# Performance work log

Hardware: AMD Instinct MI355X
Metric: run time of the kernel (lower is better)

Reference implementation:

```python
import jax, jax.numpy as jnp
import numpy as np

B, S, D, H = 8, 1024, 1024, 16
DK = D // H  # 64


def setup_inputs() -> dict:
    key = jax.random.key(0)
    ks = jax.random.split(key, 12)
    def w(k):
        return (jax.random.normal(k, (D, D), dtype=jnp.float32) * 0.02)
    def b(k):
        return (jax.random.normal(k, (D,), dtype=jnp.float32) * 0.02)
    return {
        "q": jax.random.normal(ks[0], (B, S, D), dtype=jnp.float32),
        "k": jax.random.normal(ks[1], (B, S, D), dtype=jnp.float32),
        "v": jax.random.normal(ks[2], (B, S, D), dtype=jnp.float32),
        "mask": jax.random.randint(ks[3], (B, 1, S, S), 0, 2, dtype=jnp.int32),
        "WQ_w": w(ks[4]), "WQ_b": b(ks[5]),
        "WK_w": w(ks[6]), "WK_b": b(ks[7]),
        "WV_w": w(ks[8]), "WV_b": b(ks[9]),
        "WO_w": w(ks[10]), "WO_b": b(ks[11]),
    }


def reference(q, k, v, mask, WQ_w, WQ_b, WK_w, WK_b, WV_w, WV_b, WO_w, WO_b):
    # nn.Linear: y = x @ W.T + b
    Q = (q @ WQ_w.T + WQ_b).reshape(B, S, H, DK)
    K = (k @ WK_w.T + WK_b).reshape(B, S, H, DK)
    V = (v @ WV_w.T + WV_b).reshape(B, S, H, DK)
    # scores: [B, H, Sq, Sk]
    scores = jnp.einsum("bqhd,bkhd->bhqk", Q, K) / jnp.sqrt(jnp.float32(DK))
    scores = jnp.where(mask == 0, jnp.float32(-1e9), scores)
    attn = jax.nn.softmax(scores, axis=-1)
    # dropout p=0.0 -> identity
    out = jnp.einsum("bhqk,bkhd->bqhd", attn, V).reshape(B, S, D)
    return out @ WO_w.T + WO_b
```

## Files before the change

### kernel.cpp

```cpp
#include <hip/hip_runtime.h>
#include <math.h>

typedef __bf16 bf16;
typedef __bf16 bf16x8 __attribute__((ext_vector_type(8)));
typedef __bf16 bf16x4 __attribute__((ext_vector_type(4)));
typedef float f32x2 __attribute__((ext_vector_type(2)));
typedef float f32x4 __attribute__((ext_vector_type(4)));
typedef float f32x8 __attribute__((ext_vector_type(8)));
typedef float f32x16 __attribute__((ext_vector_type(16)));
typedef int i32x2 __attribute__((ext_vector_type(2)));
typedef int i32x4 __attribute__((ext_vector_type(4)));

constexpr int B_ = 8, S_ = 1024, D_ = 1024, H_ = 16, DK_ = 64;
constexpr int M_ = B_ * S_;
constexpr size_t A8 = (size_t)1 << 23;
constexpr size_t W1 = (size_t)1 << 20;
constexpr float QSCALE = 0.18033688011112042f;

#if __has_builtin(__builtin_amdgcn_exp2f)
#define EXP2F(x) __builtin_amdgcn_exp2f(x)
#else
#define EXP2F(x) exp2f(x)
#endif
#if __has_builtin(__builtin_amdgcn_rcpf)
#define RCPF(x) __builtin_amdgcn_rcpf(x)
#else
#define RCPF(x) (1.0f / (x))
#endif

#define GAS(p) ((const __attribute__((address_space(1))) void*)(p))
#define LAS(p) ((__attribute__((address_space(3))) void*)(p))

__device__ __forceinline__ float xor32f(float v, int bpidx) {
    return __builtin_bit_cast(float,
        __builtin_amdgcn_ds_bpermute(bpidx, __builtin_bit_cast(int, v)));
}
__device__ __forceinline__ int xor32i(int v, int bpidx) {
    return __builtin_amdgcn_ds_bpermute(bpidx, v);
}
__device__ __forceinline__ int pack_bf16(bf16 lo, bf16 hi) {
    return (int)(unsigned)__builtin_bit_cast(unsigned short, lo)
         | ((int)(unsigned)__builtin_bit_cast(unsigned short, hi) << 16);
}

struct F4Q { f32x4 a, b, c, d; };

__global__ __launch_bounds__(256) void cvt_all(
    const float* __restrict__ q, const float* __restrict__ k,
    const float* __restrict__ v, const float* __restrict__ w0,
    const float* __restrict__ w1, const float* __restrict__ w2,
    const float* __restrict__ w3, bf16* __restrict__ dst)
{
    size_t e = ((size_t)blockIdx.x * 256 + threadIdx.x) * 8;
    const float* src;
    size_t off;
    if (e < 3 * A8) {
        int t = (int)(e >> 23);
        src = (t == 0) ? q : (t == 1) ? k : v;
        off = e & (A8 - 1);
    } else {
        size_t ew = e - 3 * A8;
        int t = (int)(ew >> 20);
        src = (t == 0) ? w0 : (t == 1) ? w1 : (t == 2) ? w2 : w3;
        off = ew & (W1 - 1);
    }
    float4 a = *(const float4*)(src + off);
    float4 b = *(const float4*)(src + off + 4);
    bf16x8 o = { (bf16)a.x, (bf16)a.y, (bf16)a.z, (bf16)a.w,
                 (bf16)b.x, (bf16)b.y, (bf16)b.z, (bf16)b.w };
    *(bf16x8*)(dst + e) = o;
}

__global__ __launch_bounds__(256) void mask_cvt(
    const int* __restrict__ mask, float* __restrict__ mf)
{
    const int bx = blockIdx.x;
    const int kt = bx & 15, qt = (bx >> 4) & 7, b = bx >> 7;
    const int tid = threadIdx.x;
    const int w = tid >> 6, lane = tid & 63;
    const int hi = lane >> 5, l31 = lane & 31;
    const int q = qt * 128 + w * 32 + l31;

    const int* src = mask + ((size_t)b << 20) + (size_t)q * 1024 + kt * 64 + hi * 4;
    float* dst = mf + (size_t)bx * 8192 + w * 2048 + lane * 4;
#pragma unroll
    for (int blk = 0; blk < 2; ++blk)
#pragma unroll
        for (int rr = 0; rr < 4; ++rr) {
            int4 m = *(const int4*)(src + blk * 32 + rr * 8);
            f32x4 o = { m.x ? 0.f : -1e9f, m.y ? 0.f : -1e9f,
                        m.z ? 0.f : -1e9f, m.w ? 0.f : -1e9f };
            *(f32x4*)(dst + (blk * 4 + rr) * 256) = o;
        }
}

__global__ __launch_bounds__(256) void qkv_gemm(
    const bf16* __restrict__ qb, const bf16* __restrict__ kb,
    const bf16* __restrict__ vb, const bf16* __restrict__ wq,
    const bf16* __restrict__ wk, const bf16* __restrict__ wv,
    const float* __restrict__ bq, const float* __restrict__ bk,
    const float* __restrict__ bv, bf16* __restrict__ Qp,
    bf16* __restrict__ Kp, bf16* __restrict__ Vp, float qscale)
{
    constexpr int K = 1024;
    __shared__ bf16 As[128 * 32];
    __shared__ bf16 Bs[128 * 32];

    const int bid = blockIdx.x;
    const int which = bid >> 9;
    const int gb = bid & 511;
    const bf16* X = which == 0 ? qb : which == 1 ? kb : vb;
    const bf16* W = which == 0 ? wq : which == 1 ? wk : wv;
    const float* bias = which == 0 ? bq : which == 1 ? bk : bv;
    bf16* outp = which == 0 ? Qp : which == 1 ? Kp : Vp;
    const float oscale = which == 0 ? qscale : 1.0f;

    const int tid  = threadIdx.x;
    const int lane = tid & 63;
    const int w    = tid >> 6;
    const int wm   = w & 1, wn = w >> 1;
    const int quad = lane >> 4, l15 = lane & 15;
    const int bm = (gb & 63) * 128, bn = (gb >> 6) * 128;

    f32x4 acc[4][4];
#pragma unroll
    for (int i = 0; i < 4; ++i)
#pragma unroll
        for (int j = 0; j < 4; ++j)
#pragma unroll
            for (int r = 0; r < 4; ++r) acc[i][j][r] = 0.f;

    const int lrow = lane >> 2;
    const int lcol = (lane & 3) * 8;

    for (int k0 = 0; k0 < K; k0 += 32) {
        __syncthreads();
#pragma unroll
        for (int i = 0; i < 2; ++i) {
            const int rbase = w * 16 + i * 64;
            __builtin_amdgcn_global_load_lds(
                GAS(X + (size_t)(bm + rbase + lrow) * K + k0 + lcol),
                LAS(As + rbase * 32), 16, 0, 0);
            __builtin_amdgcn_global_load_lds(
                GAS(W + (size_t)(bn + rbase + lrow) * K + k0 + lcol),
                LAS(Bs + rbase * 32), 16, 0, 0);
        }
        __syncthreads();

        bf16x8 a[4], b[4];
#pragma unroll
        for (int i = 0; i < 4; ++i)
            a[i] = *(const bf16x8*)(As + (wm * 64 + i * 16 + l15) * 32 + quad * 8);
#pragma unroll
        for (int j = 0; j < 4; ++j)
            b[j] = *(const bf16x8*)(Bs + (wn * 64 + j * 16 + l15) * 32 + quad * 8);
#pragma unroll
        for (int i = 0; i < 4; ++i)
#pragma unroll
            for (int j = 0; j < 4; ++j)
                acc[i][j] = __builtin_amdgcn_mfma_f32_16x16x32_bf16(
                    a[i], b[j], acc[i][j], 0, 0, 0);
    }

#pragma unroll
    for (int i = 0; i < 4; ++i) {
#pragma unroll
        for (int j = 0; j < 4; ++j) {
            const int n = bn + wn * 64 + j * 16 + l15;
            const float bs = bias[n];
            if (which == 2) {
                const int m0 = bm + wm * 64 + i * 16 + quad * 4;
                const int bb = m0 >> 10, s0 = m0 & 1023;
                const int h = n >> 6, dk = n & 63;
                bf16x4 o;
#pragma unroll
                for (int r = 0; r < 4; ++r) o[r] = (bf16)(acc[i][j][r] + bs);
                *(bf16x4*)(outp + (((size_t)(bb * 16 + h) * 64 + dk) << 10) + s0) = o;
            } else {
#pragma unroll
                for (int r = 0; r < 4; ++r) {
                    const int m = bm + wm * 64 + i * 16 + quad * 4 + r;
                    const int bb = m >> 10, s = m & 1023;
                    const int h = n >> 6, dk = n & 63;
                    outp[(((size_t)(bb * 16 + h)) * 1024 + s) * 64 + dk] =
                        (bf16)((acc[i][j][r] + bs) * oscale);
                }
            }
        }
    }
}

__global__ __launch_bounds__(256) void gemm_out(
    const bf16* __restrict__ X, const bf16* __restrict__ W,
    const float* __restrict__ bias, float* __restrict__ outv)
{
    constexpr int K = 1024;
    __shared__ bf16 As[128 * 32];
    __shared__ bf16 Bs[128 * 32];

    const int tid  = threadIdx.x;
    const int lane = tid & 63;
    const int w    = tid >> 6;
    const int wm   = w & 1, wn = w >> 1;
    const int quad = lane >> 4, l15 = lane & 15;
    const int bm = blockIdx.x * 128, bn = blockIdx.y * 128;

    f32x4 acc[4][4];
#pragma unroll
    for (int i = 0; i < 4; ++i)
#pragma unroll
        for (int j = 0; j < 4; ++j)
#pragma unroll
            for (int r = 0; r < 4; ++r) acc[i][j][r] = 0.f;

    const int lrow = lane >> 2;
    const int lcol = (lane & 3) * 8;

    for (int k0 = 0; k0 < K; k0 += 32) {
        __syncthreads();
#pragma unroll
        for (int i = 0; i < 2; ++i) {
            const int rbase = w * 16 + i * 64;
            __builtin_amdgcn_global_load_lds(
                GAS(X + (size_t)(bm + rbase + lrow) * K + k0 + lcol),
                LAS(As + rbase * 32), 16, 0, 0);
            __builtin_amdgcn_global_load_lds(
                GAS(W + (size_t)(bn + rbase + lrow) * K + k0 + lcol),
                LAS(Bs + rbase * 32), 16, 0, 0);
        }
        __syncthreads();

        bf16x8 a[4], b[4];
#pragma unroll
        for (int i = 0; i < 4; ++i)
            a[i] = *(const bf16x8*)(As + (wm * 64 + i * 16 + l15) * 32 + quad * 8);
#pragma unroll
        for (int j = 0; j < 4; ++j)
            b[j] = *(const bf16x8*)(Bs + (wn * 64 + j * 16 + l15) * 32 + quad * 8);
#pragma unroll
        for (int i = 0; i < 4; ++i)
#pragma unroll
            for (int j = 0; j < 4; ++j)
                acc[i][j] = __builtin_amdgcn_mfma_f32_16x16x32_bf16(
                    a[i], b[j], acc[i][j], 0, 0, 0);
    }

#pragma unroll
    for (int i = 0; i < 4; ++i)
#pragma unroll
        for (int j = 0; j < 4; ++j) {
            const int n = bn + wn * 64 + j * 16 + l15;
            const float bs = bias[n];
#pragma unroll
            for (int r = 0; r < 4; ++r) {
                const int m = bm + wm * 64 + i * 16 + quad * 4 + r;
                outv[(size_t)m * 1024 + n] = acc[i][j][r] + bs;
            }
        }
}

__global__ __launch_bounds__(256) void attn_mfma(
    const bf16* __restrict__ Q, const bf16* __restrict__ Kt,
    const bf16* __restrict__ Vt, const float* __restrict__ mf,
    bf16* __restrict__ out)
{
    __shared__ bf16 smem[2 * 2 * 4096];

    const int tid  = threadIdx.x;
    const int lane = tid & 63;
    const int w    = tid >> 6;
    const int hi   = lane >> 5, l31 = lane & 31;

    const int wid = (blockIdx.x & 7) * 128 + (blockIdx.x >> 3);
    const int qt = wid & 7;
    const int h  = (wid >> 3) & 15;
    const int b  = wid >> 7;

    const bf16* Qg  = Q + ((size_t)((b * H_ + h) * S_) + qt * 128 + w * 32) * DK_;
    const char* Kgh = (const char*)(Kt + (size_t)(b * H_ + h) * S_ * DK_);
    const char* Vgh = (const char*)(Vt + ((size_t)(b * H_ + h) << 16));
    const float* mtb = mf + (size_t)((b * 8 + qt) * 16) * 8192 + w * 2048 + lane * 4;

    const int tA = tid,        rA = tA >> 3, cA = (tA & 7) * 16;
    const int tB = 256 + tid,  rB = tB >> 3, cB = (tB & 7) * 16;
    const int kSrcA = rA * 128  + (cA ^ ((rA & 7) << 4));
    const int kSrcB = rB * 128  + (cB ^ ((rB & 7) << 4));
    const int vSrcA = rA * 2048 + (cA ^ ((rA & 7) << 4));
    const int vSrcB = rB * 2048 + (cB ^ ((rB & 7) << 4));

    auto stage = [&](int buf, int tkt) {
        bf16* Ks = smem + buf * 8192;
        bf16* Vs = Ks + 4096;
        const char* kg = Kgh + (size_t)tkt * 8192;
        const char* vg = Vgh + (size_t)tkt * 128;
        __builtin_amdgcn_global_load_lds(GAS(kg + kSrcA), LAS(Ks + w * 512),        16, 0, 0);
        __builtin_amdgcn_global_load_lds(GAS(kg + kSrcB), LAS(Ks + 2048 + w * 512), 16, 0, 0);
        __builtin_amdgcn_global_load_lds(GAS(vg + vSrcA), LAS(Vs + w * 512),        16, 0, 0);
        __builtin_amdgcn_global_load_lds(GAS(vg + vSrcB), LAS(Vs + 2048 + w * 512), 16, 0, 0);
    };

    stage(0, 0);

    bf16x8 qf[4];
#pragma unroll
    for (int ks = 0; ks < 4; ++ks)
        qf[ks] = *(const bf16x8*)(Qg + (size_t)l31 * 64 + ks * 16 + hi * 8);

    f32x4 mreg[8];
#pragma unroll
    for (int i = 0; i < 8; ++i) mreg[i] = *(const f32x4*)(mtb + i * 256);

    f32x16 O0, O1;
#pragma unroll
    for (int r = 0; r < 16; ++r) { O0[r] = 0.f; O1[r] = 0.f; }
    float mrow = -INFINITY, lrowv = 0.f;
    const int bpidx = (lane ^ 32) << 2;
    const int swz = (l31 & 7) << 4;

    __syncthreads();

#pragma unroll 2
    for (int kt = 0; kt < 16; ++kt) {
        const int buf = kt & 1;
        const bf16* Ks = smem + buf * 8192;
        const bf16* Vs = Ks + 4096;
        const char* KsB = (const char*)Ks;
        const char* VsB = (const char*)Vs;

        F4Q mq0 = { mreg[0], mreg[1], mreg[2], mreg[3] };
        F4Q mq1 = { mreg[4], mreg[5], mreg[6], mreg[7] };
        f32x16 acc0 = __builtin_bit_cast(f32x16, mq0);
        f32x16 acc1 = __builtin_bit_cast(f32x16, mq1);

        if (kt < 15) {
            const float* mkn = mtb + (size_t)(kt + 1) * 8192;
#pragma unroll
            for (int i = 0; i < 8; ++i) mreg[i] = *(const f32x4*)(mkn + i * 256);
        }

        if (kt + 1 < 16) stage(buf ^ 1, kt + 1);

        __builtin_amdgcn_s_setprio(1);
#pragma unroll
        for (int ks = 0; ks < 4; ++ks) {
            const int cb = ks * 32 + hi * 16;
            bf16x8 k0 = *(const bf16x8*)(KsB + l31 * 128        + (cb ^ swz));
            bf16x8 k1 = *(const bf16x8*)(KsB + (l31 + 32) * 128 + (cb ^ swz));
            acc0 = __builtin_amdgcn_mfma_f32_32x32x16_bf16(k0, qf[ks], acc0, 0, 0, 0);
            acc1 = __builtin_amdgcn_mfma_f32_32x32x16_bf16(k1, qf[ks], acc1, 0, 0, 0);
        }
        __builtin_amdgcn_s_setprio(0);

#if __has_builtin(__builtin_elementwise_max)
        f32x16 m16 = __builtin_elementwise_max(acc0, acc1);
        f32x8 m8 = __builtin_elementwise_max(
            __builtin_shufflevector(m16, m16, 0, 1, 2, 3, 4, 5, 6, 7),
            __builtin_shufflevector(m16, m16, 8, 9, 10, 11, 12, 13, 14, 15));
        f32x4 m4 = __builtin_elementwise_max(
            __builtin_shufflevector(m8, m8, 0, 1, 2, 3),
            __builtin_shufflevector(m8, m8, 4, 5, 6, 7));
        f32x2 m2 = __builtin_elementwise_max(
            __builtin_shufflevector(m4, m4, 0, 1),
            __builtin_shufflevector(m4, m4, 2, 3));
        float mx = fmaxf(m2[0], m2[1]);
#else
        float red[8];
#pragma unroll
        for (int i = 0; i < 8; ++i)
            red[i] = fmaxf(fmaxf(acc0[i], acc0[i + 8]), fmaxf(acc1[i], acc1[i + 8]));
#pragma unroll
        for (int i = 0; i < 4; ++i) red[i] = fmaxf(red[i], red[i + 4]);
        float mx = fmaxf(fmaxf(red[0], red[1]), fmaxf(red[2], red[3]));
#endif
        mx = fmaxf(mx, xor32f(mx, bpidx));

        if (__any(mx > mrow + 8.0f)) {
            const float mn = fmaxf(mrow, mx);
            const float alpha = EXP2F(mrow - mn);
            mrow = mn;
            lrowv *= alpha;
            O0 *= alpha;
            O1 *= alpha;
        }

        acc0 -= mrow;
        acc1 -= mrow;
#pragma unroll
        for (int r = 0; r < 16; ++r) acc0[r] = EXP2F(acc0[r]);
#pragma unroll
        for (int r = 0; r < 16; ++r) acc1[r] = EXP2F(acc1[r]);

        int wd0[8], wd1[8];
#pragma unroll
        for (int s = 0; s < 8; ++s) {
            wd0[s] = pack_bf16((bf16)acc0[2 * s], (bf16)acc0[2 * s + 1]);
            wd1[s] = pack_bf16((bf16)acc1[2 * s], (bf16)acc1[2 * s + 1]);
        }
        f32x2 ps2 = { 0.f, 0.f };
#pragma unroll
        for (int s = 0; s < 8; ++s) {
            i32x2 t0 = { wd0[s] << 16, (int)(wd0[s] & 0xffff0000) };
            i32x2 t1 = { wd1[s] << 16, (int)(wd1[s] & 0xffff0000) };
            ps2 += __builtin_bit_cast(f32x2, t0);
            ps2 += __builtin_bit_cast(f32x2, t1);
        }
        float ps = ps2[0] + ps2[1];
        ps += xor32f(ps, bpidx);
        lrowv += ps;

        __builtin_amdgcn_s_setprio(1);
#pragma unroll
        for (int ks = 0; ks < 4; ++ks) {
            const int s0 = (ks & 1) * 4;
            int p0, p1, p2, p3;
            if (ks < 2) { p0 = wd0[s0]; p1 = wd0[s0 + 1]; p2 = wd0[s0 + 2]; p3 = wd0[s0 + 3]; }
            else        { p0 = wd1[s0]; p1 = wd1[s0 + 1]; p2 = wd1[s0 + 2]; p3 = wd1[s0 + 3]; }
            const int rx = xor32i(hi ? p0 : p2, bpidx);
            const int ry = xor32i(hi ? p1 : p3, bpidx);
            i32x4 pw = { hi ? rx : p0, hi ? ry : p1, hi ? p2 : rx, hi ? p3 : ry };
            bf16x8 pa = __builtin_bit_cast(bf16x8, pw);

            const int cb = ks * 32 + hi * 16;
            bf16x8 v0 = *(const bf16x8*)(VsB + l31 * 128        + (cb ^ swz));
            bf16x8 v1 = *(const bf16x8*)(VsB + (l31 + 32) * 128 + (cb ^ swz));
            O0 = __builtin_amdgcn_mfma_f32_32x32x16_bf16(v0, pa, O0, 0, 0, 0);
            O1 = __builtin_amdgcn_mfma_f32_32x32x16_bf16(v1, pa, O1, 0, 0, 0);
        }
        __builtin_amdgcn_s_setprio(0);
        __syncthreads();
    }

    const float rinv = RCPF(lrowv);
    bf16* og = out + ((size_t)b * S_ + qt * 128 + w * 32 + l31) * D_ + h * DK_;
#pragma unroll
    for (int rr = 0; rr < 4; ++rr) {
        bf16x4 o0 = { (bf16)(O0[rr * 4 + 0] * rinv), (bf16)(O0[rr * 4 + 1] * rinv),
                      (bf16)(O0[rr * 4 + 2] * rinv), (bf16)(O0[rr * 4 + 3] * rinv) };
        bf16x4 o1 = { (bf16)(O1[rr * 4 + 0] * rinv), (bf16)(O1[rr * 4 + 1] * rinv),
                      (bf16)(O1[rr * 4 + 2] * rinv), (bf16)(O1[rr * 4 + 3] * rinv) };
        *(bf16x4*)(og + rr * 8 + hi * 4)      = o0;
        *(bf16x4*)(og + 32 + rr * 8 + hi * 4) = o1;
    }
}

extern "C" void kernel_launch(void* const* d_in, const int* in_sizes, int n_in,
                              void* d_out, int out_size, void* d_ws, size_t ws_size,
                              hipStream_t stream) {
    const float* q    = (const float*)d_in[0];
    const float* k    = (const float*)d_in[1];
    const float* v    = (const float*)d_in[2];
    const int*   mask = (const int*)d_in[3];
    const float* WQw  = (const float*)d_in[4];
    const float* WQb  = (const float*)d_in[5];
    const float* WKw  = (const float*)d_in[6];
    const float* WKb  = (const float*)d_in[7];
    const float* WVw  = (const float*)d_in[8];
    const float* WVb  = (const float*)d_in[9];
    const float* WOw  = (const float*)d_in[10];
    const float* WOb  = (const float*)d_in[11];

    bf16* ws = (bf16*)d_ws;
    bf16* qb  = ws;
    bf16* kb  = qb + A8;
    bf16* vb  = kb + A8;
    bf16* wqb = vb + A8;
    bf16* wkb = wqb + W1;
    bf16* wvb = wkb + W1;
    bf16* wob = wvb + W1;
    bf16* Qp  = wob + W1;
    bf16* Kp  = Qp + A8;
    bf16* Vp  = Kp + A8;
    float* maskf = (float*)qb;
    bf16* AO     = vb;

    cvt_all<<<dim3(14336), 256, 0, stream>>>(q, k, v, WQw, WKw, WVw, WOw, ws);

    qkv_gemm<<<dim3(1536), 256, 0, stream>>>(qb, kb, vb, wqb, wkb, wvb,
                                             WQb, WKb, WVb, Qp, Kp, Vp, QSCALE);

    mask_cvt<<<dim3(1024), 256, 0, stream>>>(mask, maskf);

    attn_mfma<<<dim3(1024), 256, 0, stream>>>(Qp, Kp, Vp, maskf, AO);

    gemm_out<<<dim3(M_ / 128, D_ / 128), 256, 0, stream>>>(AO, wob, WOb, (float*)d_out);
}
```

Measured before the change: 358.4 us.

## Fuse mask handling into attention and drop separate mask conversion kernel

Removes the standalone mask_cvt kernel, which expanded the int mask into a float additive-bias tensor. The attention kernel now loads the raw int mask per tile and multiplies the exponentiated scores by the mask cast to float, instead of seeding the QK accumulator with -1e9. This removes one kernel launch and its write-then-read of a 32 MB float buffer. In exchange, mask loads are no longer prefetched a tile ahead, and the s_setprio hints around the MFMA loops are dropped. Multiplying by the mask value matches the reference only when mask values are 0 or 1, and a fully masked row would give NaN instead of a uniform softmax.

Result: no change. 361.5 us (+0.9%).

```diff
diff --git a/kernel.cpp b/kernel.cpp
--- a/kernel.cpp
+++ b/kernel.cpp
@@ -71,29 +71,6 @@
     *(bf16x8*)(dst + e) = o;
 }
 
-__global__ __launch_bounds__(256) void mask_cvt(
-    const int* __restrict__ mask, float* __restrict__ mf)
-{
-    const int bx = blockIdx.x;
-    const int kt = bx & 15, qt = (bx >> 4) & 7, b = bx >> 7;
-    const int tid = threadIdx.x;
-    const int w = tid >> 6, lane = tid & 63;
-    const int hi = lane >> 5, l31 = lane & 31;
-    const int q = qt * 128 + w * 32 + l31;
-
-    const int* src = mask + ((size_t)b << 20) + (size_t)q * 1024 + kt * 64 + hi * 4;
-    float* dst = mf + (size_t)bx * 8192 + w * 2048 + lane * 4;
-#pragma unroll
-    for (int blk = 0; blk < 2; ++blk)
-#pragma unroll
-        for (int rr = 0; rr < 4; ++rr) {
-            int4 m = *(const int4*)(src + blk * 32 + rr * 8);
-            f32x4 o = { m.x ? 0.f : -1e9f, m.y ? 0.f : -1e9f,
-                        m.z ? 0.f : -1e9f, m.w ? 0.f : -1e9f };
-            *(f32x4*)(dst + (blk * 4 + rr) * 256) = o;
-        }
-}
-
 __global__ __launch_bounds__(256) void qkv_gemm(
     const bf16* __restrict__ qb, const bf16* __restrict__ kb,
     const bf16* __restrict__ vb, const bf16* __restrict__ wq,
@@ -261,7 +238,7 @@
 
 __global__ __launch_bounds__(256) void attn_mfma(
     const bf16* __restrict__ Q, const bf16* __restrict__ Kt,
-    const bf16* __restrict__ Vt, const float* __restrict__ mf,
+    const bf16* __restrict__ Vt, const int* __restrict__ mask,
     bf16* __restrict__ out)
 {
     __shared__ bf16 smem[2 * 2 * 4096];
@@ -279,7 +256,8 @@
     const bf16* Qg  = Q + ((size_t)((b * H_ + h) * S_) + qt * 128 + w * 32) * DK_;
     const char* Kgh = (const char*)(Kt + (size_t)(b * H_ + h) * S_ * DK_);
     const char* Vgh = (const char*)(Vt + ((size_t)(b * H_ + h) << 16));
-    const float* mtb = mf + (size_t)((b * 8 + qt) * 16) * 8192 + w * 2048 + lane * 4;
+    const int* mrp = mask + ((size_t)b << 20)
+                   + (size_t)(qt * 128 + w * 32 + l31) * 1024 + hi * 4;
 
     const int tA = tid,        rA = tA >> 3, cA = (tA & 7) * 16;
     const int tB = 256 + tid,  rB = tB >> 3, cB = (tB & 7) * 16;
@@ -306,10 +284,6 @@
     for (int ks = 0; ks < 4; ++ks)
         qf[ks] = *(const bf16x8*)(Qg + (size_t)l31 * 64 + ks * 16 + hi * 8);
 
-    f32x4 mreg[8];
-#pragma unroll
-    for (int i = 0; i < 8; ++i) mreg[i] = *(const f32x4*)(mtb + i * 256);
-
     f32x16 O0, O1;
 #pragma unroll
     for (int r = 0; r < 16; ++r) { O0[r] = 0.f; O1[r] = 0.f; }
@@ -327,20 +301,18 @@
         const char* KsB = (const char*)Ks;
         const char* VsB = (const char*)Vs;
 
-        F4Q mq0 = { mreg[0], mreg[1], mreg[2], mreg[3] };
-        F4Q mq1 = { mreg[4], mreg[5], mreg[6], mreg[7] };
-        f32x16 acc0 = __builtin_bit_cast(f32x16, mq0);
-        f32x16 acc1 = __builtin_bit_cast(f32x16, mq1);
-
-        if (kt < 15) {
-            const float* mkn = mtb + (size_t)(kt + 1) * 8192;
-#pragma unroll
-            for (int i = 0; i < 8; ++i) mreg[i] = *(const f32x4*)(mkn + i * 256);
+        int4 mi[8];
+#pragma unroll
+        for (int rr = 0; rr < 4; ++rr) {
+            mi[rr]     = *(const int4*)(mrp + kt * 64 + rr * 8);
+            mi[rr + 4] = *(const int4*)(mrp + kt * 64 + 32 + rr * 8);
         }
 
         if (kt + 1 < 16) stage(buf ^ 1, kt + 1);
 
-        __builtin_amdgcn_s_setprio(1);
+        f32x16 acc0, acc1;
+#pragma unroll
+        for (int r = 0; r < 16; ++r) { acc0[r] = 0.f; acc1[r] = 0.f; }
 #pragma unroll
         for (int ks = 0; ks < 4; ++ks) {
             const int cb = ks * 32 + hi * 16;
@@ -349,7 +321,6 @@
             acc0 = __builtin_amdgcn_mfma_f32_32x32x16_bf16(k0, qf[ks], acc0, 0, 0, 0);
             acc1 = __builtin_amdgcn_mfma_f32_32x32x16_bf16(k1, qf[ks], acc1, 0, 0, 0);
         }
-        __builtin_amdgcn_s_setprio(0);
 
 #if __has_builtin(__builtin_elementwise_max)
         f32x16 m16 = __builtin_elementwise_max(acc0, acc1);
@@ -390,6 +361,16 @@
 #pragma unroll
         for (int r = 0; r < 16; ++r) acc1[r] = EXP2F(acc1[r]);
 
+        f32x4 mv[8];
+#pragma unroll
+        for (int i = 0; i < 8; ++i)
+            mv[i] = (f32x4){ (float)mi[i].x, (float)mi[i].y,
+                             (float)mi[i].z, (float)mi[i].w };
+        F4Q mm0 = { mv[0], mv[1], mv[2], mv[3] };
+        F4Q mm1 = { mv[4], mv[5], mv[6], mv[7] };
+        acc0 *= __builtin_bit_cast(f32x16, mm0);
+        acc1 *= __builtin_bit_cast(f32x16, mm1);
+
         int wd0[8], wd1[8];
 #pragma unroll
         for (int s = 0; s < 8; ++s) {
@@ -408,7 +389,6 @@
         ps += xor32f(ps, bpidx);
         lrowv += ps;
 
-        __builtin_amdgcn_s_setprio(1);
 #pragma unroll
         for (int ks = 0; ks < 4; ++ks) {
             const int s0 = (ks & 1) * 4;
@@ -426,7 +406,6 @@
             O0 = __builtin_amdgcn_mfma_f32_32x32x16_bf16(v0, pa, O0, 0, 0, 0);
             O1 = __builtin_amdgcn_mfma_f32_32x32x16_bf16(v1, pa, O1, 0, 0, 0);
         }
-        __builtin_amdgcn_s_setprio(0);
         __syncthreads();
     }
 
@@ -470,17 +449,14 @@
     bf16* Qp  = wob + W1;
     bf16* Kp  = Qp + A8;
     bf16* Vp  = Kp + A8;
-    float* maskf = (float*)qb;
-    bf16* AO     = vb;
+    bf16* AO  = vb;
 
     cvt_all<<<dim3(14336), 256, 0, stream>>>(q, k, v, WQw, WKw, WVw, WOw, ws);
 
     qkv_gemm<<<dim3(1536), 256, 0, stream>>>(qb, kb, vb, wqb, wkb, wvb,
                                              WQb, WKb, WVb, Qp, Kp, Vp, QSCALE);
 
-    mask_cvt<<<dim3(1024), 256, 0, stream>>>(mask, maskf);
-
-    attn_mfma<<<dim3(1024), 256, 0, stream>>>(Qp, Kp, Vp, maskf, AO);
+    attn_mfma<<<dim3(1024), 256, 0, stream>>>(Qp, Kp, Vp, mask, AO);
 
     gemm_out<<<dim3(M_ / 128, D_ / 128), 256, 0, stream>>>(AO, wob, WOb, (float*)d_out);
 }
```
